# Optimization experiments

Measured on AMD Instinct MI355X. Metric: run time of the kernel, lower is better.

## Reference

```python
import jax, jax.numpy as jnp
import numpy as np

N_NODES = 50000
N_EDGES = 800000
IN_SIZE = 128
NUM_HEADS = 8
HEAD_DIM = IN_SIZE // NUM_HEADS  # qk/val head dim = 16


def setup_inputs() -> dict:
    key = jax.random.key(0)
    ks = jax.random.split(key, 16)
    d = IN_SIZE
    lim = 1.0 / np.sqrt(d)
    inp = {
        "in_feats": jax.random.normal(ks[0], (N_NODES, d), jnp.float32),
        "struc_feats": jax.random.normal(ks[1], (N_NODES, d), jnp.float32),
        "edge_weights": jax.random.uniform(ks[2], (N_EDGES,), jnp.float32),
        "ln_scale": jnp.ones((d,), jnp.float32),
        "ln_bias": jnp.zeros((d,), jnp.float32),
        "Ws": jax.random.uniform(ks[3], (d, d), jnp.float32, -lim, lim),
        "bs": jnp.zeros((d,), jnp.float32),
        "Wq": jax.random.uniform(ks[4], (d, d), jnp.float32, -lim, lim),
        "bq": jnp.zeros((d,), jnp.float32),
        "Wk": jax.random.uniform(ks[5], (d, d), jnp.float32, -lim, lim),
        "bk": jnp.zeros((d,), jnp.float32),
        "Wv": jax.random.uniform(ks[6], (d, d), jnp.float32, -lim, lim),
        "bv": jnp.zeros((d,), jnp.float32),
        "Wo": jax.random.uniform(ks[7], (d, d), jnp.float32, -lim, lim),
        "edge_ids": jax.random.randint(ks[8], (2, N_EDGES), 0, N_NODES, jnp.int64)
        if jax.config.jax_enable_x64 else jax.random.randint(ks[8], (2, N_EDGES), 0, N_NODES, jnp.int32),
    }
    return inp


def _layer_norm(x, scale, bias, eps=1e-5):
    mu = jnp.mean(x, axis=-1, keepdims=True)
    var = jnp.var(x, axis=-1, keepdims=True)
    return (x - mu) * jax.lax.rsqrt(var + eps) * scale + bias


def reference(in_feats, struc_feats, edge_weights, ln_scale, ln_bias,
              Ws, bs, Wq, bq, Wk, bk, Wv, bv, Wo, edge_ids):
    N = in_feats.shape[0]
    H, hd = NUM_HEADS, HEAD_DIM

    delta = _layer_norm(in_feats, ln_scale, ln_bias)           # pre-norm
    delta = jax.nn.gelu(delta, approximate=False)               # pre-activation (exact GELU, torch default)
    delta_struc = delta + struc_feats @ Ws.T + bs               # struc_proj add

    qry = (delta_struc @ Wq.T + bq) / np.sqrt(hd)                # [N, qk]
    keyf = delta_struc @ Wk.T + bk                               # [N, qk]
    val = delta @ Wv.T + bv                                      # [N, val]

    src, dst = edge_ids[0], edge_ids[1]                          # out[src] += A[src,dst] * val[dst]
    qe = qry[src].reshape(-1, H, hd)                             # [E, H, hd]
    ke = keyf[dst].reshape(-1, H, hd)                            # [E, H, hd]
    attn = jax.nn.sigmoid(jnp.sum(qe * ke, axis=-1))             # [E, H]
    attn = edge_weights[:, None] * attn

    msgs = attn[:, :, None] * val[dst].reshape(-1, H, hd)        # [E, H, hd]
    agg = jax.ops.segment_sum(msgs.reshape(-1, H * hd), src, num_segments=N)  # [N, val]

    out = agg @ Wo.T                                             # out_proj (no bias)
    return in_feats + out                                        # skip connection
```

## Files before the change

### kernel.cpp

```cpp
#include <hip/hip_runtime.h>
#include <math.h>

#define NF 128

typedef __attribute__((ext_vector_type(8))) short short8;
typedef __attribute__((ext_vector_type(4))) float floatx4;

__device__ __forceinline__ unsigned short f2bf(float f) {
    union { float x; unsigned int i; } c; c.x = f;
    unsigned int r = c.i + 0x7fffu + ((c.i >> 16) & 1u);
    return (unsigned short)(r >> 16);
}
__device__ __forceinline__ float bf2f(unsigned short u) {
    union { unsigned int i; float x; } c; c.i = ((unsigned int)u) << 16;
    return c.x;
}
__device__ __forceinline__ void unpack8(uint4 u, float* f) {
    union { unsigned int i; float x; } c;
    c.i = u.x << 16;          f[0] = c.x;
    c.i = u.x & 0xffff0000u;  f[1] = c.x;
    c.i = u.y << 16;          f[2] = c.x;
    c.i = u.y & 0xffff0000u;  f[3] = c.x;
    c.i = u.z << 16;          f[4] = c.x;
    c.i = u.z & 0xffff0000u;  f[5] = c.x;
    c.i = u.w << 16;          f[6] = c.x;
    c.i = u.w & 0xffff0000u;  f[7] = c.x;
}
__device__ __forceinline__ ushort4 pack4(float a, float b, float c, float d) {
    ushort4 h; h.x = f2bf(a); h.y = f2bf(b); h.z = f2bf(c); h.w = f2bf(d);
    return h;
}

__global__ __launch_bounds__(256) void wconv_hist_kernel(
    const float* __restrict__ a, const float* __restrict__ b,
    const float* __restrict__ c, const float* __restrict__ d,
    const float* __restrict__ e, unsigned short* __restrict__ o,
    const int* __restrict__ eid, int* __restrict__ cnt,
    int* __restrict__ rank, int E)
{
    int blk = blockIdx.x;
    if (blk < 320) {
        int i = blk * 256 + threadIdx.x;
        int w = i >> 14, j = i & 16383;
        const float* p = (w == 0) ? a : (w == 1) ? b : (w == 2) ? c : (w == 3) ? d : e;
        o[i] = f2bf(p[j]);
    } else {
        int i = (blk - 320) * 256 + threadIdx.x;
        if (i < E) rank[i] = atomicAdd(&cnt[eid[i]], 1);
    }
}

__global__ __launch_bounds__(256) void scan1_kernel(
    const int* __restrict__ cnt, int* __restrict__ bsum, int n)
{
    int base = blockIdx.x * 1024;
    int s = 0;
    #pragma unroll
    for (int p = 0; p < 4; ++p) {
        int i = base + (int)threadIdx.x + p * 256;
        if (i < n) s += cnt[i];
    }
    #pragma unroll
    for (int m = 1; m <= 32; m <<= 1) s += __shfl_xor(s, m, 64);
    __shared__ int ws_[4];
    int wid = threadIdx.x >> 6;
    if ((threadIdx.x & 63) == 0) ws_[wid] = s;
    __syncthreads();
    if (threadIdx.x == 0) bsum[blockIdx.x] = ws_[0] + ws_[1] + ws_[2] + ws_[3];
}

__global__ __launch_bounds__(256) void scan3_ln_kernel(
    const int* __restrict__ cnt, const int* __restrict__ bsum,
    int* __restrict__ row_start, int n, int nb,
    const float* __restrict__ in_feats, const float* __restrict__ gamma,
    const float* __restrict__ beta, unsigned short* __restrict__ deltab, int M)
{
    int blk = blockIdx.x;
    if (blk < nb) {
        __shared__ int base_off;
        int tid = threadIdx.x, lane = tid & 63, wid = tid >> 6;
        if (tid == 0) {
            int a = 0;
            for (int j = 0; j < blk; ++j) a += bsum[j];
            base_off = a;
            if (blk == nb - 1) {
                int tot = a;
                for (int j = blk; j < nb; ++j) tot += bsum[j];
                row_start[n] = tot;
            }
        }
        int base = blk * 1024;
        int v[4]; int s = 0;
        #pragma unroll
        for (int p = 0; p < 4; ++p) {
            int i = base + tid * 4 + p;
            v[p] = (i < n) ? cnt[i] : 0;
            s += v[p];
        }
        int ss = s;
        #pragma unroll
        for (int off = 1; off < 64; off <<= 1) {
            int t = __shfl_up(ss, off, 64);
            if (lane >= off) ss += t;
        }
        __shared__ int wsum[4];
        if (lane == 63) wsum[wid] = ss;
        __syncthreads();
        int woff = 0;
        for (int j = 0; j < wid; ++j) woff += wsum[j];
        int a = base_off + woff + (ss - s);
        #pragma unroll
        for (int p = 0; p < 4; ++p) {
            int i = base + tid * 4 + p;
            if (i < n) { row_start[i] = a; a += v[p]; }
        }
        return;
    }
    int li = (blk - nb) * 256 + threadIdx.x;
    int row = li >> 2, t4 = li & 3;
    if (row >= M) return;
    size_t rbase = (size_t)row * NF;

    const float4* ip = (const float4*)(in_feats + rbase) + t4 * 8;
    float4 xf[8];
    #pragma unroll
    for (int p = 0; p < 8; ++p) xf[p] = ip[p];
    float s = 0.f, sq = 0.f;
    #pragma unroll
    for (int p = 0; p < 8; ++p) {
        s  += xf[p].x + xf[p].y + xf[p].z + xf[p].w;
        sq += xf[p].x * xf[p].x + xf[p].y * xf[p].y
            + xf[p].z * xf[p].z + xf[p].w * xf[p].w;
    }
    s  += __shfl_xor(s, 1, 64);  s  += __shfl_xor(s, 2, 64);
    sq += __shfl_xor(sq, 1, 64); sq += __shfl_xor(sq, 2, 64);
    float mu = s * (1.0f / 128.0f);
    float var = sq * (1.0f / 128.0f) - mu * mu;
    float rstd = rsqrtf(var + 1e-5f);

    const float4* gp = (const float4*)gamma + t4 * 8;
    const float4* bp = (const float4*)beta + t4 * 8;
    uint dreg[16];
    #pragma unroll
    for (int p = 0; p < 8; ++p) {
        float4 g4 = gp[p], b4 = bp[p];
        float o0 = (xf[p].x - mu) * rstd * g4.x + b4.x;
        float o1 = (xf[p].y - mu) * rstd * g4.y + b4.y;
        float o2 = (xf[p].z - mu) * rstd * g4.z + b4.z;
        float o3 = (xf[p].w - mu) * rstd * g4.w + b4.w;
        o0 = 0.5f * o0 * (1.0f + erff(o0 * 0.70710678118654752f));
        o1 = 0.5f * o1 * (1.0f + erff(o1 * 0.70710678118654752f));
        o2 = 0.5f * o2 * (1.0f + erff(o2 * 0.70710678118654752f));
        o3 = 0.5f * o3 * (1.0f + erff(o3 * 0.70710678118654752f));
        ushort4 h = pack4(o0, o1, o2, o3);
        dreg[p * 2]     = (uint)h.x | ((uint)h.y << 16);
        dreg[p * 2 + 1] = (uint)h.z | ((uint)h.w << 16);
    }
    uint4* od = (uint4*)(deltab + rbase + t4 * 32);
    #pragma unroll
    for (int q = 0; q < 4; ++q)
        od[q] = make_uint4(dreg[q*4], dreg[q*4+1], dreg[q*4+2], dreg[q*4+3]);
}

__global__ __launch_bounds__(256) void scatter_dv_kernel(
    const int* __restrict__ eid, const float* __restrict__ ew,
    const int* __restrict__ row_start, const int* __restrict__ rank,
    int2* __restrict__ edata, int E, int sb,
    const float* __restrict__ struc, const unsigned short* __restrict__ deltab,
    const unsigned short* __restrict__ Wall, const float* __restrict__ bs,
    const float* __restrict__ bv, unsigned short* __restrict__ dstrb,
    unsigned short* __restrict__ kvb, int M, int nt, int ndv)
{
    __shared__ unsigned short Wl[128][136];
    __shared__ unsigned short Cst[64][136];

    int blk = blockIdx.x;
    if (blk < sb) {
        int i = blk * 256 + threadIdx.x;
        if (i < E) {
            int src = eid[i];
            int pos = row_start[src] + rank[i];
            edata[pos] = make_int2(eid[E + i], __float_as_int(ew[i]));
        }
        return;
    }

    int idx = blk - sb;
    int y = idx / ndv;
    int xb = idx % ndv;

    int tid = threadIdx.x;
    int lane = tid & 63, w = tid >> 6, lg = lane & 15, quad = lane >> 4;

    const unsigned short* Wg = Wall + ((y == 0) ? 0 : 3 * 16384);
    const float* bias = (y == 0) ? bs : bv;
    unsigned short* outg = (y == 0) ? dstrb : (kvb + NF);
    int ostride = (y == 0) ? NF : 2 * NF;

    {
        const uint4* g = (const uint4*)Wg;
        #pragma unroll
        for (int p = 0; p < 8; ++p) {
            int i2 = tid + p * 256;
            *(uint4*)&Wl[i2 >> 4][(i2 & 15) * 8] = g[i2];
        }
    }
    float br[8];
    #pragma unroll
    for (int t = 0; t < 8; ++t) br[t] = bias[t * 16 + lg];
    __syncthreads();

    for (int tile = xb; tile < nt; tile += ndv) {
        int m0 = tile * 64;
        int am = m0 + w * 16 + lg;
        size_t rb = (size_t)(am < M ? am : 0) * NF;

        short8 af[4];
        if (y == 0) {
            const float4* sp = (const float4*)(struc + rb);
            #pragma unroll
            for (int ks = 0; ks < 4; ++ks) {
                float4 f0 = sp[ks * 8 + quad * 2];
                float4 f1 = sp[ks * 8 + quad * 2 + 1];
                ushort4 h0 = pack4(f0.x, f0.y, f0.z, f0.w);
                ushort4 h1 = pack4(f1.x, f1.y, f1.z, f1.w);
                uint4 pk = make_uint4((uint)h0.x | ((uint)h0.y << 16),
                                      (uint)h0.z | ((uint)h0.w << 16),
                                      (uint)h1.x | ((uint)h1.y << 16),
                                      (uint)h1.z | ((uint)h1.w << 16));
                af[ks] = *(short8*)&pk;
            }
        } else {
            const unsigned short* arow = deltab + rb + quad * 8;
            #pragma unroll
            for (int ks = 0; ks < 4; ++ks) af[ks] = *(const short8*)(arow + ks * 32);
        }

        floatx4 acc[8];
        #pragma unroll
        for (int t = 0; t < 8; ++t) acc[t] = (floatx4){0.f, 0.f, 0.f, 0.f};
        #pragma unroll
        for (int ks = 0; ks < 4; ++ks) {
            #pragma unroll
            for (int t = 0; t < 8; ++t) {
                short8 b = *(const short8*)&Wl[t * 16 + lg][ks * 32 + quad * 8];
                acc[t] = __builtin_amdgcn_mfma_f32_16x16x32_bf16(af[ks], b, acc[t], 0, 0, 0);
            }
        }

        if (y == 0) {
            #pragma unroll
            for (int t = 0; t < 8; ++t) {
                int col = t * 16 + lg;
                #pragma unroll
                for (int r = 0; r < 4; ++r) {
                    int gm = m0 + w * 16 + quad * 4 + r;
                    float dadd = bf2f(deltab[(size_t)(gm < M ? gm : 0) * NF + col]);
                    Cst[w * 16 + quad * 4 + r][col] = f2bf(acc[t][r] + br[t] + dadd);
                }
            }
        } else {
            #pragma unroll
            for (int t = 0; t < 8; ++t) {
                int col = t * 16 + lg;
                #pragma unroll
                for (int r = 0; r < 4; ++r)
                    Cst[w * 16 + quad * 4 + r][col] = f2bf(acc[t][r] + br[t]);
            }
        }
        #pragma unroll
        for (int p = 0; p < 4; ++p) {
            int i2 = lane + p * 64;
            int row = w * 16 + (i2 >> 4), c16 = i2 & 15;
            int gm = m0 + row;
            if (gm < M)
                *(uint4*)(outg + (size_t)gm * ostride + c16 * 8) = *(const uint4*)&Cst[row][c16 * 8];
        }
    }
}

__global__ __launch_bounds__(256) void gemm_qk_kernel(
    const unsigned short* __restrict__ dstrb, const unsigned short* __restrict__ Wall,
    const float* __restrict__ bq, const float* __restrict__ bk,
    unsigned short* __restrict__ qb, unsigned short* __restrict__ kvb,
    int M, int nt)
{
    __shared__ unsigned short Wl[128][136];
    __shared__ unsigned short Cst[64][136];

    int tid = threadIdx.x;
    int y = blockIdx.y;
    int lane = tid & 63, w = tid >> 6, lg = lane & 15, quad = lane >> 4;

    const unsigned short* Wg = Wall + (y + 1) * 16384;
    const float* bias = (y == 0) ? bq : bk;
    float scale = (y == 0) ? 0.25f : 1.0f;
    unsigned short* outg = (y == 0) ? qb : kvb;
    int ostride = (y == 0) ? NF : 2 * NF;

    {
        const uint4* g = (const uint4*)Wg;
        #pragma unroll
        for (int p = 0; p < 8; ++p) {
            int idx = tid + p * 256;
            *(uint4*)&Wl[idx >> 4][(idx & 15) * 8] = g[idx];
        }
    }
    float br[8];
    #pragma unroll
    for (int t = 0; t < 8; ++t) br[t] = bias[t * 16 + lg] * scale;
    __syncthreads();

    for (int tile = blockIdx.x; tile < nt; tile += gridDim.x) {
        int m0 = tile * 64;
        int am = m0 + w * 16 + lg;
        const unsigned short* arow = dstrb + (size_t)(am < M ? am : 0) * NF + quad * 8;

        floatx4 acc[8];
        #pragma unroll
        for (int t = 0; t < 8; ++t) acc[t] = (floatx4){0.f, 0.f, 0.f, 0.f};
        short8 af[4];
        #pragma unroll
        for (int ks = 0; ks < 4; ++ks) af[ks] = *(const short8*)(arow + ks * 32);
        #pragma unroll
        for (int ks = 0; ks < 4; ++ks) {
            #pragma unroll
            for (int t = 0; t < 8; ++t) {
                short8 b = *(const short8*)&Wl[t * 16 + lg][ks * 32 + quad * 8];
                acc[t] = __builtin_amdgcn_mfma_f32_16x16x32_bf16(af[ks], b, acc[t], 0, 0, 0);
            }
        }
        #pragma unroll
        for (int t = 0; t < 8; ++t) {
            int col = t * 16 + lg;
            #pragma unroll
            for (int r = 0; r < 4; ++r)
                Cst[w * 16 + quad * 4 + r][col] = f2bf(acc[t][r] * scale + br[t]);
        }
        #pragma unroll
        for (int p = 0; p < 4; ++p) {
            int idx = lane + p * 64;
            int row = w * 16 + (idx >> 4), c16 = idx & 15;
            int gm = m0 + row;
            if (gm < M)
                *(uint4*)(outg + (size_t)gm * ostride + c16 * 8) = *(const uint4*)&Cst[row][c16 * 8];
        }
    }
}

__global__ __launch_bounds__(256) void gemm_out_kernel(
    const unsigned short* __restrict__ Xb, const unsigned short* __restrict__ Wb,
    const float* __restrict__ addf, float* __restrict__ Y, int M, int nt)
{
    __shared__ unsigned short Wl[128][136];
    int tid = threadIdx.x;
    int lane = tid & 63, w = tid >> 6, lg = lane & 15, quad = lane >> 4;

    {
        const uint4* g = (const uint4*)Wb;
        #pragma unroll
        for (int p = 0; p < 8; ++p) {
            int idx = tid + p * 256;
            *(uint4*)&Wl[idx >> 4][(idx & 15) * 8] = g[idx];
        }
    }
    __syncthreads();

    for (int tile = blockIdx.x; tile < nt; tile += gridDim.x) {
        int m0 = tile * 64;
        int am = m0 + w * 16 + lg;
        const unsigned short* arow = Xb + (size_t)(am < M ? am : 0) * NF + quad * 8;

        floatx4 acc[8];
        #pragma unroll
        for (int t = 0; t < 8; ++t) acc[t] = (floatx4){0.f, 0.f, 0.f, 0.f};
        short8 af[4];
        #pragma unroll
        for (int ks = 0; ks < 4; ++ks) af[ks] = *(const short8*)(arow + ks * 32);
        #pragma unroll
        for (int ks = 0; ks < 4; ++ks) {
            #pragma unroll
            for (int t = 0; t < 8; ++t) {
                short8 b = *(const short8*)&Wl[t * 16 + lg][ks * 32 + quad * 8];
                acc[t] = __builtin_amdgcn_mfma_f32_16x16x32_bf16(af[ks], b, acc[t], 0, 0, 0);
            }
        }
        #pragma unroll
        for (int t = 0; t < 8; ++t) {
            int col = t * 16 + lg;
            #pragma unroll
            for (int r = 0; r < 4; ++r) {
                int gm = m0 + w * 16 + quad * 4 + r;
                if (gm >= M) continue;
                size_t off = (size_t)gm * NF + col;
                Y[off] = acc[t][r] + addf[off];
            }
        }
    }
}

__global__ __launch_bounds__(256) void aggregate_kernel(
    const unsigned short* __restrict__ Q, const unsigned short* __restrict__ kvb,
    const int* __restrict__ row_start, const int2* __restrict__ edata,
    unsigned short* __restrict__ agg, int N)
{
    int node = blockIdx.x * 4 + (threadIdx.x >> 6);
    if (node >= N) return;
    int lane = threadIdx.x & 63;
    int sg = lane >> 4, lg = lane & 15;
    int rs = row_start[node], re = row_start[node + 1];

    float qv[8];
    unpack8(*(const uint4*)(Q + (size_t)node * NF + lg * 8), qv);
    float acc[8];
    #pragma unroll
    for (int j = 0; j < 8; ++j) acc[j] = 0.f;

    int e1 = rs + sg, e2 = rs + sg + 4;
    int2 ed1 = (e1 < re) ? edata[e1] : make_int2(0, 0);
    int2 ed2 = (e2 < re) ? edata[e2] : make_int2(0, 0);

    for (int e0 = rs; e0 < re; e0 += 8) {
        int2 c1 = ed1, c2 = ed2;
        int en1 = e0 + 8 + sg, en2 = en1 + 4;
        ed1 = (en1 < re) ? edata[en1] : make_int2(0, 0);
        ed2 = (en2 < re) ? edata[en2] : make_int2(0, 0);

        const uint4* p1 = (const uint4*)kvb + (size_t)c1.x * 32 + lg;
        const uint4* p2 = (const uint4*)kvb + (size_t)c2.x * 32 + lg;
        uint4 k1u = p1[0], v1u = p1[16];
        uint4 k2u = p2[0], v2u = p2[16];

        float kv1[8], kv2[8];
        unpack8(k1u, kv1);
        unpack8(k2u, kv2);
        float s1 = qv[0] * kv1[0], s2 = qv[0] * kv2[0];
        #pragma unroll
        for (int j = 1; j < 8; ++j) {
            s1 = fmaf(qv[j], kv1[j], s1);
            s2 = fmaf(qv[j], kv2[j], s2);
        }
        s1 += __shfl_xor(s1, 1, 64);
        s2 += __shfl_xor(s2, 1, 64);
        float a1 = __int_as_float(c1.y) / (1.f + __expf(-s1));
        float a2 = __int_as_float(c2.y) / (1.f + __expf(-s2));

        float vv1[8], vv2[8];
        unpack8(v1u, vv1);
        unpack8(v2u, vv2);
        #pragma unroll
        for (int j = 0; j < 8; ++j) {
            acc[j] = fmaf(a1, vv1[j], acc[j]);
            acc[j] = fmaf(a2, vv2[j], acc[j]);
        }
    }
    #pragma unroll
    for (int j = 0; j < 8; ++j) {
        acc[j] += __shfl_xor(acc[j], 16, 64);
        acc[j] += __shfl_xor(acc[j], 32, 64);
    }
    if (sg == 0) {
        unsigned short* o = agg + (size_t)node * NF + lg * 8;
        *(ushort4*)o       = pack4(acc[0], acc[1], acc[2], acc[3]);
        *(ushort4*)(o + 4) = pack4(acc[4], acc[5], acc[6], acc[7]);
    }
}

extern "C" void kernel_launch(void* const* d_in, const int* in_sizes, int n_in,
                              void* d_out, int out_size, void* d_ws, size_t ws_size,
                              hipStream_t stream)
{
    const float* in_feats = (const float*)d_in[0];
    const float* struc    = (const float*)d_in[1];
    const float* eweights = (const float*)d_in[2];
    const float* ln_scale = (const float*)d_in[3];
    const float* ln_bias  = (const float*)d_in[4];
    const float* Ws       = (const float*)d_in[5];
    const float* bs       = (const float*)d_in[6];
    const float* Wq       = (const float*)d_in[7];
    const float* bq       = (const float*)d_in[8];
    const float* Wk       = (const float*)d_in[9];
    const float* bk       = (const float*)d_in[10];
    const float* Wv       = (const float*)d_in[11];
    const float* bv       = (const float*)d_in[12];
    const float* Wo       = (const float*)d_in[13];
    const int*   edge_ids = (const int*)d_in[14];
    float* out = (float*)d_out;

    int N = in_sizes[0] / NF;
    int E = in_sizes[2];

    size_t F = (size_t)N * NF;
    unsigned short* deltab = (unsigned short*)d_ws;
    unsigned short* dstrb  = deltab + F;
    unsigned short* qb     = dstrb + F;
    unsigned short* kvb    = qb + F;
    unsigned short* aggb   = kvb + 2 * F;
    unsigned short* Wall   = aggb + F;
    int2*  edata     = (int2*)(Wall + 5 * 16384);
    int*   cnt       = (int*)(edata + E);
    int*   row_start = cnt + N;
    int*   bsum      = row_start + N + 1;
    int*   rank      = bsum + 64;

    int nt  = (N + 63) / 64;
    int geb = (E + 255) / 256;
    int nb  = (N + 1023) / 1024;
    int ppb = (N * 4 + 255) / 256;
    int ndv = 261;

    hipMemsetAsync(cnt, 0, (size_t)N * sizeof(int), stream);
    wconv_hist_kernel<<<320 + geb, 256, 0, stream>>>(Ws, Wq, Wk, Wv, Wo, Wall,
                                                     edge_ids, cnt, rank, E);

    scan1_kernel<<<nb, 256, 0, stream>>>(cnt, bsum, N);

    scan3_ln_kernel<<<nb + ppb, 256, 0, stream>>>(cnt, bsum, row_start, N, nb,
                                                  in_feats, ln_scale, ln_bias,
                                                  deltab, N);

    scatter_dv_kernel<<<geb + 2 * ndv, 256, 0, stream>>>(edge_ids, eweights,
                                                         row_start, rank, edata, E, geb,
                                                         struc, deltab, Wall, bs, bv,
                                                         dstrb, kvb, N, nt, ndv);

    gemm_qk_kernel<<<dim3(261, 2), 256, 0, stream>>>(dstrb, Wall, bq, bk,
                                                     qb, kvb, N, nt);

    aggregate_kernel<<<(N + 3) / 4, 256, 0, stream>>>(qb, kvb, row_start, edata, aggb, N);

    gemm_out_kernel<<<nt, 256, 0, stream>>>(aggb, Wall + 4 * 16384, in_feats, out, N, nt);
}
```

Measured before the change: 290.6 us.

## Drop LDS weight staging and use one tile per block in projection GEMMs

The projection GEMM kernels (struc/V and Q/K) no longer stage the 128x128 bf16 weight matrix in shared memory. Each MFMA B fragment is now read directly from global memory, relying on the L1/L2 caches. The persistent grid-stride loop over 261 blocks is replaced by one 64-row tile per block, launching nt blocks per projection. This removes the per-block weight copy and barrier and lowers LDS use, which may raise occupancy, but every block now fetches the weights from global memory instead of reusing an LDS copy across many tiles.

Measured after the change: 329.9 us. +13.5%, slower.

```diff
diff --git a/kernel.cpp b/kernel.cpp
--- a/kernel.cpp
+++ b/kernel.cpp
@@ -169,9 +169,8 @@
     const float* __restrict__ struc, const unsigned short* __restrict__ deltab,
     const unsigned short* __restrict__ Wall, const float* __restrict__ bs,
     const float* __restrict__ bv, unsigned short* __restrict__ dstrb,
-    unsigned short* __restrict__ kvb, int M, int nt, int ndv)
-{
-    __shared__ unsigned short Wl[128][136];
+    unsigned short* __restrict__ kvb, int M, int nt)
+{
     __shared__ unsigned short Cst[64][136];
 
     int blk = blockIdx.x;
@@ -186,8 +185,8 @@
     }
 
     int idx = blk - sb;
-    int y = idx / ndv;
-    int xb = idx % ndv;
+    int y = idx / nt;
+    int tile = idx % nt;
 
     int tid = threadIdx.x;
     int lane = tid & 63, w = tid >> 6, lg = lane & 15, quad = lane >> 4;
@@ -197,85 +196,74 @@
     unsigned short* outg = (y == 0) ? dstrb : (kvb + NF);
     int ostride = (y == 0) ? NF : 2 * NF;
 
-    {
-        const uint4* g = (const uint4*)Wg;
-        #pragma unroll
-        for (int p = 0; p < 8; ++p) {
-            int i2 = tid + p * 256;
-            *(uint4*)&Wl[i2 >> 4][(i2 & 15) * 8] = g[i2];
-        }
-    }
     float br[8];
     #pragma unroll
     for (int t = 0; t < 8; ++t) br[t] = bias[t * 16 + lg];
-    __syncthreads();
-
-    for (int tile = xb; tile < nt; tile += ndv) {
-        int m0 = tile * 64;
-        int am = m0 + w * 16 + lg;
-        size_t rb = (size_t)(am < M ? am : 0) * NF;
-
-        short8 af[4];
-        if (y == 0) {
-            const float4* sp = (const float4*)(struc + rb);
+
+    int m0 = tile * 64;
+    int am = m0 + w * 16 + lg;
+    size_t rb = (size_t)(am < M ? am : 0) * NF;
+
+    short8 af[4];
+    if (y == 0) {
+        const float4* sp = (const float4*)(struc + rb);
+        #pragma unroll
+        for (int ks = 0; ks < 4; ++ks) {
+            float4 f0 = sp[ks * 8 + quad * 2];
+            float4 f1 = sp[ks * 8 + quad * 2 + 1];
+            ushort4 h0 = pack4(f0.x, f0.y, f0.z, f0.w);
+            ushort4 h1 = pack4(f1.x, f1.y, f1.z, f1.w);
+            uint4 pk = make_uint4((uint)h0.x | ((uint)h0.y << 16),
+                                  (uint)h0.z | ((uint)h0.w << 16),
+                                  (uint)h1.x | ((uint)h1.y << 16),
+                                  (uint)h1.z | ((uint)h1.w << 16));
+            af[ks] = *(short8*)&pk;
+        }
+    } else {
+        const unsigned short* arow = deltab + rb + quad * 8;
+        #pragma unroll
+        for (int ks = 0; ks < 4; ++ks) af[ks] = *(const short8*)(arow + ks * 32);
+    }
+
+    floatx4 acc[8];
+    #pragma unroll
+    for (int t = 0; t < 8; ++t) acc[t] = (floatx4){0.f, 0.f, 0.f, 0.f};
+    #pragma unroll
+    for (int ks = 0; ks < 4; ++ks) {
+        #pragma unroll
+        for (int t = 0; t < 8; ++t) {
+            short8 b = *(const short8*)(Wg + ((t * 16 + lg) << 7) + ks * 32 + quad * 8);
+            acc[t] = __builtin_amdgcn_mfma_f32_16x16x32_bf16(af[ks], b, acc[t], 0, 0, 0);
+        }
+    }
+
+    if (y == 0) {
+        #pragma unroll
+        for (int t = 0; t < 8; ++t) {
+            int col = t * 16 + lg;
             #pragma unroll
-            for (int ks = 0; ks < 4; ++ks) {
-                float4 f0 = sp[ks * 8 + quad * 2];
-                float4 f1 = sp[ks * 8 + quad * 2 + 1];
-                ushort4 h0 = pack4(f0.x, f0.y, f0.z, f0.w);
-                ushort4 h1 = pack4(f1.x, f1.y, f1.z, f1.w);
-                uint4 pk = make_uint4((uint)h0.x | ((uint)h0.y << 16),
-                                      (uint)h0.z | ((uint)h0.w << 16),
-                                      (uint)h1.x | ((uint)h1.y << 16),
-                                      (uint)h1.z | ((uint)h1.w << 16));
-                af[ks] = *(short8*)&pk;
+            for (int r = 0; r < 4; ++r) {
+                int gm = m0 + w * 16 + quad * 4 + r;
+                float dadd = bf2f(deltab[(size_t)(gm < M ? gm : 0) * NF + col]);
+                Cst[w * 16 + quad * 4 + r][col] = f2bf(acc[t][r] + br[t] + dadd);
             }
-        } else {
-            const unsigned short* arow = deltab + rb + quad * 8;
+        }
+    } else {
+        #pragma unroll
+        for (int t = 0; t < 8; ++t) {
+            int col = t * 16 + lg;
             #pragma unroll
-            for (int ks = 0; ks < 4; ++ks) af[ks] = *(const short8*)(arow + ks * 32);
-        }
-
-        floatx4 acc[8];
-        #pragma unroll
-        for (int t = 0; t < 8; ++t) acc[t] = (floatx4){0.f, 0.f, 0.f, 0.f};
-        #pragma unroll
-        for (int ks = 0; ks < 4; ++ks) {
-            #pragma unroll
-            for (int t = 0; t < 8; ++t) {
-                short8 b = *(const short8*)&Wl[t * 16 + lg][ks * 32 + quad * 8];
-                acc[t] = __builtin_amdgcn_mfma_f32_16x16x32_bf16(af[ks], b, acc[t], 0, 0, 0);
-            }
-        }
-
-        if (y == 0) {
-            #pragma unroll
-            for (int t = 0; t < 8; ++t) {
-                int col = t * 16 + lg;
-                #pragma unroll
-                for (int r = 0; r < 4; ++r) {
-                    int gm = m0 + w * 16 + quad * 4 + r;
-                    float dadd = bf2f(deltab[(size_t)(gm < M ? gm : 0) * NF + col]);
-                    Cst[w * 16 + quad * 4 + r][col] = f2bf(acc[t][r] + br[t] + dadd);
-                }
-            }
-        } else {
-            #pragma unroll
-            for (int t = 0; t < 8; ++t) {
-                int col = t * 16 + lg;
-                #pragma unroll
-                for (int r = 0; r < 4; ++r)
-                    Cst[w * 16 + quad * 4 + r][col] = f2bf(acc[t][r] + br[t]);
-            }
-        }
-        #pragma unroll
-        for (int p = 0; p < 4; ++p) {
-            int i2 = lane + p * 64;
-            int row = w * 16 + (i2 >> 4), c16 = i2 & 15;
-            int gm = m0 + row;
-            if (gm < M)
-                *(uint4*)(outg + (size_t)gm * ostride + c16 * 8) = *(const uint4*)&Cst[row][c16 * 8];
-        }
+            for (int r = 0; r < 4; ++r)
+                Cst[w * 16 + quad * 4 + r][col] = f2bf(acc[t][r] + br[t]);
+        }
+    }
+    #pragma unroll
+    for (int p = 0; p < 4; ++p) {
+        int i2 = lane + p * 64;
+        int row = w * 16 + (i2 >> 4), c16 = i2 & 15;
+        int gm = m0 + row;
+        if (gm < M)
+            *(uint4*)(outg + (size_t)gm * ostride + c16 * 8) = *(const uint4*)&Cst[row][c16 * 8];
     }
 }
 
@@ -285,7 +273,6 @@
     unsigned short* __restrict__ qb, unsigned short* __restrict__ kvb,
     int M, int nt)
 {
-    __shared__ unsigned short Wl[128][136];
     __shared__ unsigned short Cst[64][136];
 
     int tid = threadIdx.x;
@@ -298,53 +285,44 @@
     unsigned short* outg = (y == 0) ? qb : kvb;
     int ostride = (y == 0) ? NF : 2 * NF;
 
-    {
-        const uint4* g = (const uint4*)Wg;
-        #pragma unroll
-        for (int p = 0; p < 8; ++p) {
-            int idx = tid + p * 256;
-            *(uint4*)&Wl[idx >> 4][(idx & 15) * 8] = g[idx];
-        }
-    }
     float br[8];
     #pragma unroll
     for (int t = 0; t < 8; ++t) br[t] = bias[t * 16 + lg] * scale;
-    __syncthreads();
-
-    for (int tile = blockIdx.x; tile < nt; tile += gridDim.x) {
-        int m0 = tile * 64;
-        int am = m0 + w * 16 + lg;
-        const unsigned short* arow = dstrb + (size_t)(am < M ? am : 0) * NF + quad * 8;
-
-        floatx4 acc[8];
-        #pragma unroll
-        for (int t = 0; t < 8; ++t) acc[t] = (floatx4){0.f, 0.f, 0.f, 0.f};
-        short8 af[4];
-        #pragma unroll
-        for (int ks = 0; ks < 4; ++ks) af[ks] = *(const short8*)(arow + ks * 32);
-        #pragma unroll
-        for (int ks = 0; ks < 4; ++ks) {
-            #pragma unroll
-            for (int t = 0; t < 8; ++t) {
-                short8 b = *(const short8*)&Wl[t * 16 + lg][ks * 32 + quad * 8];
-                acc[t] = __builtin_amdgcn_mfma_f32_16x16x32_bf16(af[ks], b, acc[t], 0, 0, 0);
-            }
-        }
+
+    int tile = blockIdx.x;
+    if (tile >= nt) return;
+    int m0 = tile * 64;
+    int am = m0 + w * 16 + lg;
+    const unsigned short* arow = dstrb + (size_t)(am < M ? am : 0) * NF + quad * 8;
+
+    floatx4 acc[8];
+    #pragma unroll
+    for (int t = 0; t < 8; ++t) acc[t] = (floatx4){0.f, 0.f, 0.f, 0.f};
+    short8 af[4];
+    #pragma unroll
+    for (int ks = 0; ks < 4; ++ks) af[ks] = *(const short8*)(arow + ks * 32);
+    #pragma unroll
+    for (int ks = 0; ks < 4; ++ks) {
         #pragma unroll
         for (int t = 0; t < 8; ++t) {
-            int col = t * 16 + lg;
-            #pragma unroll
-            for (int r = 0; r < 4; ++r)
-                Cst[w * 16 + quad * 4 + r][col] = f2bf(acc[t][r] * scale + br[t]);
-        }
-        #pragma unroll
-        for (int p = 0; p < 4; ++p) {
-            int idx = lane + p * 64;
-            int row = w * 16 + (idx >> 4), c16 = idx & 15;
-            int gm = m0 + row;
-            if (gm < M)
-                *(uint4*)(outg + (size_t)gm * ostride + c16 * 8) = *(const uint4*)&Cst[row][c16 * 8];
-        }
+            short8 b = *(const short8*)(Wg + ((t * 16 + lg) << 7) + ks * 32 + quad * 8);
+            acc[t] = __builtin_amdgcn_mfma_f32_16x16x32_bf16(af[ks], b, acc[t], 0, 0, 0);
+        }
+    }
+    #pragma unroll
+    for (int t = 0; t < 8; ++t) {
+        int col = t * 16 + lg;
+        #pragma unroll
+        for (int r = 0; r < 4; ++r)
+            Cst[w * 16 + quad * 4 + r][col] = f2bf(acc[t][r] * scale + br[t]);
+    }
+    #pragma unroll
+    for (int p = 0; p < 4; ++p) {
+        int idx = lane + p * 64;
+        int row = w * 16 + (idx >> 4), c16 = idx & 15;
+        int gm = m0 + row;
+        if (gm < M)
+            *(uint4*)(outg + (size_t)gm * ostride + c16 * 8) = *(const uint4*)&Cst[row][c16 * 8];
     }
 }
 
@@ -507,7 +485,6 @@
     int geb = (E + 255) / 256;
     int nb  = (N + 1023) / 1024;
     int ppb = (N * 4 + 255) / 256;
-    int ndv = 261;
 
     hipMemsetAsync(cnt, 0, (size_t)N * sizeof(int), stream);
     wconv_hist_kernel<<<320 + geb, 256, 0, stream>>>(Ws, Wq, Wk, Wv, Wo, Wall,
@@ -519,13 +496,13 @@
                                                   in_feats, ln_scale, ln_bias,
                                                   deltab, N);
 
-    scatter_dv_kernel<<<geb + 2 * ndv, 256, 0, stream>>>(edge_ids, eweights,
-                                                         row_start, rank, edata, E, geb,
-                                                         struc, deltab, Wall, bs, bv,
-                                                         dstrb, kvb, N, nt, ndv);
-
-    gemm_qk_kernel<<<dim3(261, 2), 256, 0, stream>>>(dstrb, Wall, bq, bk,
-                                                     qb, kvb, N, nt);
+    scatter_dv_kernel<<<geb + 2 * nt, 256, 0, stream>>>(edge_ids, eweights,
+                                                        row_start, rank, edata, E, geb,
+                                                        struc, deltab, Wall, bs, bv,
+                                                        dstrb, kvb, N, nt);
+
+    gemm_qk_kernel<<<dim3(nt, 2), 256, 0, stream>>>(dstrb, Wall, bq, bk,
+                                                    qb, kvb, N, nt);
 
     aggregate_kernel<<<(N + 3) / 4, 256, 0, stream>>>(qb, kvb, row_start, edata, aggb, N);
 
```

## Fuse output projection GEMM into the edge aggregation kernel

Applied to the files above, without the earlier changes.

The separate out-projection GEMM kernel is removed and its work moves into the end of the per-node aggregation kernel. Each wave shuffles its aggregated row into bf16 MFMA operands, multiplies by Wo loaded straight from global memory, and writes the output with the residual add. This drops the bf16 intermediate round trip through memory and one kernel launch. In exchange, every wave re-reads the full Wo matrix from cache, and the 16x16 MFMA tiles are mostly redundant because only one node row is real.

Result: slower. 446.1 us (+53.5%).

```diff
diff --git a/kernel.cpp b/kernel.cpp
--- a/kernel.cpp
+++ b/kernel.cpp
@@ -348,61 +348,11 @@
     }
 }
 
-__global__ __launch_bounds__(256) void gemm_out_kernel(
-    const unsigned short* __restrict__ Xb, const unsigned short* __restrict__ Wb,
-    const float* __restrict__ addf, float* __restrict__ Y, int M, int nt)
-{
-    __shared__ unsigned short Wl[128][136];
-    int tid = threadIdx.x;
-    int lane = tid & 63, w = tid >> 6, lg = lane & 15, quad = lane >> 4;
-
-    {
-        const uint4* g = (const uint4*)Wb;
-        #pragma unroll
-        for (int p = 0; p < 8; ++p) {
-            int idx = tid + p * 256;
-            *(uint4*)&Wl[idx >> 4][(idx & 15) * 8] = g[idx];
-        }
-    }
-    __syncthreads();
-
-    for (int tile = blockIdx.x; tile < nt; tile += gridDim.x) {
-        int m0 = tile * 64;
-        int am = m0 + w * 16 + lg;
-        const unsigned short* arow = Xb + (size_t)(am < M ? am : 0) * NF + quad * 8;
-
-        floatx4 acc[8];
-        #pragma unroll
-        for (int t = 0; t < 8; ++t) acc[t] = (floatx4){0.f, 0.f, 0.f, 0.f};
-        short8 af[4];
-        #pragma unroll
-        for (int ks = 0; ks < 4; ++ks) af[ks] = *(const short8*)(arow + ks * 32);
-        #pragma unroll
-        for (int ks = 0; ks < 4; ++ks) {
-            #pragma unroll
-            for (int t = 0; t < 8; ++t) {
-                short8 b = *(const short8*)&Wl[t * 16 + lg][ks * 32 + quad * 8];
-                acc[t] = __builtin_amdgcn_mfma_f32_16x16x32_bf16(af[ks], b, acc[t], 0, 0, 0);
-            }
-        }
-        #pragma unroll
-        for (int t = 0; t < 8; ++t) {
-            int col = t * 16 + lg;
-            #pragma unroll
-            for (int r = 0; r < 4; ++r) {
-                int gm = m0 + w * 16 + quad * 4 + r;
-                if (gm >= M) continue;
-                size_t off = (size_t)gm * NF + col;
-                Y[off] = acc[t][r] + addf[off];
-            }
-        }
-    }
-}
-
-__global__ __launch_bounds__(256) void aggregate_kernel(
+__global__ __launch_bounds__(256) void aggregate_out_kernel(
     const unsigned short* __restrict__ Q, const unsigned short* __restrict__ kvb,
     const int* __restrict__ row_start, const int2* __restrict__ edata,
-    unsigned short* __restrict__ agg, int N)
+    const unsigned short* __restrict__ Wo4, const float* __restrict__ in_feats,
+    float* __restrict__ out, int N)
 {
     int node = blockIdx.x * 4 + (threadIdx.x >> 6);
     if (node >= N) return;
@@ -459,10 +409,38 @@
         acc[j] += __shfl_xor(acc[j], 16, 64);
         acc[j] += __shfl_xor(acc[j], 32, 64);
     }
+
+    floatx4 po[8];
+    #pragma unroll
+    for (int t = 0; t < 8; ++t) po[t] = (floatx4){0.f, 0.f, 0.f, 0.f};
+    #pragma unroll
+    for (int ks = 0; ks < 4; ++ks) {
+        float f0 = __shfl(acc[0], ks * 4 + sg, 64);
+        float f1 = __shfl(acc[1], ks * 4 + sg, 64);
+        float f2 = __shfl(acc[2], ks * 4 + sg, 64);
+        float f3 = __shfl(acc[3], ks * 4 + sg, 64);
+        float f4 = __shfl(acc[4], ks * 4 + sg, 64);
+        float f5 = __shfl(acc[5], ks * 4 + sg, 64);
+        float f6 = __shfl(acc[6], ks * 4 + sg, 64);
+        float f7 = __shfl(acc[7], ks * 4 + sg, 64);
+        uint4 pk = make_uint4((uint)f2bf(f0) | ((uint)f2bf(f1) << 16),
+                              (uint)f2bf(f2) | ((uint)f2bf(f3) << 16),
+                              (uint)f2bf(f4) | ((uint)f2bf(f5) << 16),
+                              (uint)f2bf(f6) | ((uint)f2bf(f7) << 16));
+        short8 a = *(short8*)&pk;
+        #pragma unroll
+        for (int t = 0; t < 8; ++t) {
+            short8 b = *(const short8*)(Wo4 + ((t * 16 + lg) << 7) + ks * 32 + sg * 8);
+            po[t] = __builtin_amdgcn_mfma_f32_16x16x32_bf16(a, b, po[t], 0, 0, 0);
+        }
+    }
     if (sg == 0) {
-        unsigned short* o = agg + (size_t)node * NF + lg * 8;
-        *(ushort4*)o       = pack4(acc[0], acc[1], acc[2], acc[3]);
-        *(ushort4*)(o + 4) = pack4(acc[4], acc[5], acc[6], acc[7]);
+        size_t ob = (size_t)node * NF;
+        #pragma unroll
+        for (int t = 0; t < 8; ++t) {
+            int c = t * 16 + lg;
+            out[ob + c] = po[t][0] + in_feats[ob + c];
+        }
     }
 }
 
@@ -495,8 +473,7 @@
     unsigned short* dstrb  = deltab + F;
     unsigned short* qb     = dstrb + F;
     unsigned short* kvb    = qb + F;
-    unsigned short* aggb   = kvb + 2 * F;
-    unsigned short* Wall   = aggb + F;
+    unsigned short* Wall   = kvb + 2 * F;
     int2*  edata     = (int2*)(Wall + 5 * 16384);
     int*   cnt       = (int*)(edata + E);
     int*   row_start = cnt + N;
@@ -527,7 +504,7 @@
     gemm_qk_kernel<<<dim3(261, 2), 256, 0, stream>>>(dstrb, Wall, bq, bk,
                                                      qb, kvb, N, nt);
 
-    aggregate_kernel<<<(N + 3) / 4, 256, 0, stream>>>(qb, kvb, row_start, edata, aggb, N);
-
-    gemm_out_kernel<<<nt, 256, 0, stream>>>(aggb, Wall + 4 * 16384, in_feats, out, N, nt);
-}
+    aggregate_out_kernel<<<(N + 3) / 4, 256, 0, stream>>>(qb, kvb, row_start, edata,
+                                                          Wall + 4 * 16384,
+                                                          in_feats, out, N);
+}
```
